# Kernel optimization log

Hardware: AMD Instinct MI355X
Metric: run time of the kernel (lower is better)

Reference implementation:

```python
import jax, jax.numpy as jnp
import numpy as np

B, N, D = 4, 1024, 1024
NH = 16
HS = D // NH
HID = 4 * D
EPS = 1e-5

def layernorm(x, w, b):
    mu = jnp.mean(x, axis=-1, keepdims=True)
    var = jnp.mean(jnp.square(x - mu), axis=-1, keepdims=True)
    return (x - mu) * jax.lax.rsqrt(var + EPS) * w + b

def setup_inputs() -> dict:
    key = jax.random.key(0)
    ks = jax.random.split(key, 8)
    s = lambda fan_in: 1.0 / np.sqrt(fan_in)
    return {
        "x": jax.random.normal(ks[0], (B, N, D), jnp.float32),
        "qkv_w": jax.random.uniform(ks[1], (3 * D, D), jnp.float32, -s(D), s(D)),
        "proj_w": jax.random.uniform(ks[2], (D, D), jnp.float32, -s(D), s(D)),
        "proj_b": jax.random.uniform(ks[3], (D,), jnp.float32, -s(D), s(D)),
        "ln1_w": jnp.ones((D,), jnp.float32),
        "ln1_b": jnp.zeros((D,), jnp.float32),
        "fc1_w": jax.random.uniform(ks[4], (HID, D), jnp.float32, -s(D), s(D)),
        "fc1_b": jax.random.uniform(ks[5], (HID,), jnp.float32, -s(D), s(D)),
        "fc2_w": jax.random.uniform(ks[6], (D, HID), jnp.float32, -s(HID), s(HID)),
        "fc2_b": jax.random.uniform(ks[7], (D,), jnp.float32, -s(HID), s(HID)),
        "ln2_w": jnp.ones((D,), jnp.float32),
        "ln2_b": jnp.zeros((D,), jnp.float32),
    }

def attention(x, qkv_w, proj_w, proj_b):
    # x: [b, n, d]; qkv linear (no bias), split into q,k,v per head
    qkv = jnp.einsum('bnd,ed->bne', x, qkv_w)              # [b, n, 3d]
    qkv = qkv.reshape(B, N, 3, NH, HS).transpose(2, 0, 3, 1, 4)  # [3, b, nh, n, hs]
    q, k, v = qkv[0], qkv[1], qkv[2]
    scale = HS ** -0.5
    # mask=False => self.mask == 1, so (mask-1)*LARGE_NUMBER == 0
    att = jax.nn.softmax(scale * jnp.einsum('bhqe,bhke->bhqk', q, k), axis=-1)
    y = jnp.einsum('bhqk,bhke->bhqe', att, v)              # [b, nh, n, hs]
    y = y.transpose(0, 2, 1, 3).reshape(B, N, D)
    return jnp.einsum('bnd,ed->bne', y, proj_w) + proj_b

def mlp(x, fc1_w, fc1_b, fc2_w, fc2_b):
    h = jax.nn.gelu(jnp.einsum('bnd,hd->bnh', x, fc1_w) + fc1_b, approximate=False)
    return jnp.einsum('bnh,dh->bnd', h, fc2_w) + fc2_b

def reference(x, qkv_w, proj_w, proj_b, ln1_w, ln1_b, fc1_w, fc1_b, fc2_w, fc2_b, ln2_w, ln2_b):
    x = x + attention(layernorm(x, ln1_w, ln1_b), qkv_w, proj_w, proj_b)
    x = x + mlp(layernorm(x, ln2_w, ln2_b), fc1_w, fc1_b, fc2_w, fc2_b)
    return x
```

## Files before the change

kernel.cpp:

```cpp
#include <hip/hip_runtime.h>
#include <hip/hip_bf16.h>

typedef __attribute__((ext_vector_type(8))) short short8;
typedef __attribute__((ext_vector_type(8))) unsigned short ushort8;
typedef __attribute__((ext_vector_type(4))) float floatx4;

#define DEV static __device__ __forceinline__

DEV unsigned short f2bf(float f) {
  unsigned int u = __builtin_bit_cast(unsigned int, f);
  u += 0x7fff + ((u >> 16) & 1);
  return (unsigned short)(u >> 16);
}
DEV float bf2f(unsigned short u) {
  return __builtin_bit_cast(float, (unsigned int)u << 16);
}
DEV unsigned int cvtpk_bf16(float lo, float hi) {
  unsigned int r;
  asm("v_cvt_pk_bf16_f32 %0, %1, %2" : "=v"(r) : "v"(lo), "v"(hi));
  return r;
}

DEV void gload_lds16(const void* g, void* l) {
  __builtin_amdgcn_global_load_lds(
      (const __attribute__((address_space(1))) unsigned int*)g,
      (__attribute__((address_space(3))) unsigned int*)l, 16, 0, 0);
}

__global__ __launch_bounds__(256) void cvt4_kernel(const float* __restrict__ w0,
                                                   const float* __restrict__ w1,
                                                   const float* __restrict__ w2,
                                                   const float* __restrict__ w3,
                                                   unsigned short* __restrict__ o0,
                                                   unsigned short* __restrict__ o1,
                                                   unsigned short* __restrict__ o2,
                                                   unsigned short* __restrict__ o3) {
  int i = blockIdx.x * 256 + threadIdx.x;
  const float* in; unsigned short* out; int j;
  if (i < 786432)       { in = w0; out = o0; j = i; }
  else if (i < 1048576) { in = w1; out = o1; j = i - 786432; }
  else if (i < 2097152) { in = w2; out = o2; j = i - 1048576; }
  else                  { in = w3; out = o3; j = i - 2097152; }
  float4 v = reinterpret_cast<const float4*>(in)[j];
  ushort4 o;
  o.x = f2bf(v.x); o.y = f2bf(v.y); o.z = f2bf(v.z); o.w = f2bf(v.w);
  reinterpret_cast<ushort4*>(out)[j] = o;
}

__global__ __launch_bounds__(256) void ln_kernel(const float* __restrict__ x,
                                                 const float* __restrict__ w,
                                                 const float* __restrict__ b,
                                                 unsigned short* __restrict__ out) {
  const int row = blockIdx.x;
  const float* xr = x + (size_t)row * 1024;
  float4 v = reinterpret_cast<const float4*>(xr)[threadIdx.x];
  float s  = v.x + v.y + v.z + v.w;
  float ss = v.x*v.x + v.y*v.y + v.z*v.z + v.w*v.w;
  #pragma unroll
  for (int off = 1; off < 64; off <<= 1) {
    s  += __shfl_xor(s, off);
    ss += __shfl_xor(ss, off);
  }
  __shared__ float red[8];
  const int wid = threadIdx.x >> 6, lane = threadIdx.x & 63;
  if (lane == 0) { red[wid] = s; red[4 + wid] = ss; }
  __syncthreads();
  s  = red[0] + red[1] + red[2] + red[3];
  ss = red[4] + red[5] + red[6] + red[7];
  const float mu  = s * (1.0f / 1024.0f);
  const float var = ss * (1.0f / 1024.0f) - mu * mu;
  const float rstd = rsqrtf(var + 1e-5f);
  float4 wv = reinterpret_cast<const float4*>(w)[threadIdx.x];
  float4 bv = reinterpret_cast<const float4*>(b)[threadIdx.x];
  ushort4 o;
  o.x = f2bf((v.x - mu) * rstd * wv.x + bv.x);
  o.y = f2bf((v.y - mu) * rstd * wv.y + bv.y);
  o.z = f2bf((v.z - mu) * rstd * wv.z + bv.z);
  o.w = f2bf((v.w - mu) * rstd * wv.w + bv.w);
  reinterpret_cast<ushort4*>(out)[(size_t)row * 256 + threadIdx.x] = o;
}

template<int EPI>
__global__ __launch_bounds__(512, 2) void gemm256(const unsigned short* __restrict__ A,
                                                  const unsigned short* __restrict__ Bw,
                                                  unsigned short* __restrict__ outb,
                                                  const float* __restrict__ bias,
                                                  int K, int N, int NT) {
  __shared__ unsigned short As[2][256 * 64];
  __shared__ unsigned short Bs[2][256 * 64];
  const int tid = threadIdx.x, lane = tid & 63, wid = tid >> 6;
  const int wr = wid >> 2, wc = wid & 3;
  const int fr = lane & 15, s0 = lane >> 4;

  const int nwg = gridDim.x;
  const int qq = nwg >> 3, rr8 = nwg & 7, xcd = blockIdx.x & 7, lid = blockIdx.x >> 3;
  const int wg = (xcd < rr8 ? xcd * (qq + 1) : rr8 * (qq + 1) + (xcd - rr8) * qq) + lid;
  const int brow = (wg / NT) * 256, bcol = (wg % NT) * 256;

  const unsigned short* ag[4];
  const unsigned short* bg[4];
  #pragma unroll
  for (int L = 0; L < 4; L++) {
    const int idx = L * 512 + tid;
    const int row = idx >> 3;
    const int ss  = ((idx & 7) ^ (row & 7)) * 8;
    ag[L] = A  + (size_t)(brow + row) * K + ss;
    bg[L] = Bw + (size_t)(bcol + row) * K + ss;
  }
  const int ldst = tid * 8;

  #define STG256(kt, buf)                                                     \
    do {                                                                      \
      const int ko = (kt) * 64;                                               \
      gload_lds16(ag[0] + ko, &As[buf][ldst]);                                \
      gload_lds16(ag[1] + ko, &As[buf][4096 + ldst]);                         \
      gload_lds16(ag[2] + ko, &As[buf][8192 + ldst]);                         \
      gload_lds16(ag[3] + ko, &As[buf][12288 + ldst]);                        \
      gload_lds16(bg[0] + ko, &Bs[buf][ldst]);                                \
      gload_lds16(bg[1] + ko, &Bs[buf][4096 + ldst]);                         \
      gload_lds16(bg[2] + ko, &Bs[buf][8192 + ldst]);                         \
      gload_lds16(bg[3] + ko, &Bs[buf][12288 + ldst]);                        \
    } while (0)

  const int xs = fr & 7;
  const int aoff = (wr * 128 + fr) * 64;
  const int boff = (wc * 64 + fr) * 64;
  const int sl0 = ((0 + s0) ^ xs) * 8;
  const int sl1 = ((4 + s0) ^ xs) * 8;

  floatx4 acc[8][4];
  #pragma unroll
  for (int m = 0; m < 8; m++)
    #pragma unroll
    for (int n = 0; n < 4; n++) acc[m][n] = (floatx4){0.f, 0.f, 0.f, 0.f};

  const int NTK = K >> 6;
  STG256(0, 0);

  for (int kt = 0; kt < NTK; ++kt) {
    const int cur = kt & 1;
    if (kt + 1 < NTK) {
      STG256(kt + 1, cur ^ 1);
      asm volatile("s_waitcnt vmcnt(8)" ::: "memory");
    } else {
      asm volatile("s_waitcnt vmcnt(0)" ::: "memory");
    }
    __builtin_amdgcn_s_barrier();

    const unsigned short* Ac = As[cur];
    const unsigned short* Bc = Bs[cur];
    short8 a0[4][2], a1[4][2], b0[2][2], b1[2][2];

    #pragma unroll
    for (int m = 0; m < 4; m++) {
      a0[m][0] = *reinterpret_cast<const short8*>(Ac + aoff + m * 1024 + sl0);
      a0[m][1] = *reinterpret_cast<const short8*>(Ac + aoff + m * 1024 + sl1);
    }
    #pragma unroll
    for (int n = 0; n < 2; n++) {
      b0[n][0] = *reinterpret_cast<const short8*>(Bc + boff + n * 1024 + sl0);
      b0[n][1] = *reinterpret_cast<const short8*>(Bc + boff + n * 1024 + sl1);
    }
    __builtin_amdgcn_s_barrier();
    __builtin_amdgcn_s_setprio(1);
    #pragma unroll
    for (int m = 0; m < 4; m++)
      #pragma unroll
      for (int n = 0; n < 2; n++) {
        acc[m][n] = __builtin_amdgcn_mfma_f32_16x16x32_bf16(a0[m][0], b0[n][0], acc[m][n], 0, 0, 0);
        acc[m][n] = __builtin_amdgcn_mfma_f32_16x16x32_bf16(a0[m][1], b0[n][1], acc[m][n], 0, 0, 0);
      }
    __builtin_amdgcn_s_setprio(0);
    __builtin_amdgcn_s_barrier();

    #pragma unroll
    for (int n = 0; n < 2; n++) {
      b1[n][0] = *reinterpret_cast<const short8*>(Bc + boff + (n + 2) * 1024 + sl0);
      b1[n][1] = *reinterpret_cast<const short8*>(Bc + boff + (n + 2) * 1024 + sl1);
    }
    __builtin_amdgcn_s_barrier();
    __builtin_amdgcn_s_setprio(1);
    #pragma unroll
    for (int m = 0; m < 4; m++)
      #pragma unroll
      for (int n = 0; n < 2; n++) {
        acc[m][n + 2] = __builtin_amdgcn_mfma_f32_16x16x32_bf16(a0[m][0], b1[n][0], acc[m][n + 2], 0, 0, 0);
        acc[m][n + 2] = __builtin_amdgcn_mfma_f32_16x16x32_bf16(a0[m][1], b1[n][1], acc[m][n + 2], 0, 0, 0);
      }
    __builtin_amdgcn_s_setprio(0);
    __builtin_amdgcn_s_barrier();

    #pragma unroll
    for (int m = 0; m < 4; m++) {
      a1[m][0] = *reinterpret_cast<const short8*>(Ac + aoff + (m + 4) * 1024 + sl0);
      a1[m][1] = *reinterpret_cast<const short8*>(Ac + aoff + (m + 4) * 1024 + sl1);
    }
    __builtin_amdgcn_s_barrier();
    __builtin_amdgcn_s_setprio(1);
    #pragma unroll
    for (int m = 0; m < 4; m++)
      #pragma unroll
      for (int n = 0; n < 2; n++) {
        acc[m + 4][n] = __builtin_amdgcn_mfma_f32_16x16x32_bf16(a1[m][0], b0[n][0], acc[m + 4][n], 0, 0, 0);
        acc[m + 4][n] = __builtin_amdgcn_mfma_f32_16x16x32_bf16(a1[m][1], b0[n][1], acc[m + 4][n], 0, 0, 0);
      }
    __builtin_amdgcn_s_setprio(0);
    __builtin_amdgcn_s_barrier();

    __builtin_amdgcn_s_setprio(1);
    #pragma unroll
    for (int m = 0; m < 4; m++)
      #pragma unroll
      for (int n = 0; n < 2; n++) {
        acc[m + 4][n + 2] = __builtin_amdgcn_mfma_f32_16x16x32_bf16(a1[m][0], b1[n][0], acc[m + 4][n + 2], 0, 0, 0);
        acc[m + 4][n + 2] = __builtin_amdgcn_mfma_f32_16x16x32_bf16(a1[m][1], b1[n][1], acc[m + 4][n + 2], 0, 0, 0);
      }
    __builtin_amdgcn_s_setprio(0);
    __builtin_amdgcn_s_barrier();
  }
  #undef STG256

  #pragma unroll
  for (int m = 0; m < 8; m++) {
    #pragma unroll
    for (int n = 0; n < 4; n++) {
      const int col = bcol + wc * 64 + n * 16 + fr;
      #pragma unroll
      for (int r = 0; r < 4; r++) {
        const size_t idx = (size_t)(brow + wr * 128 + m * 16 + s0 * 4 + r) * N + col;
        float v = acc[m][n][r];
        if (EPI == 1) {
          v += bias[col];
          const float u = v * 0.7978845608f * (1.0f + 0.044715f * v * v);
          const float e = __expf(2.0f * u);
          v = v * (e / (e + 1.0f));
        }
        outb[idx] = f2bf(v);
      }
    }
  }
}

__global__ __launch_bounds__(512) void gemm128sk(const unsigned short* __restrict__ A,
                                                 const unsigned short* __restrict__ Bw,
                                                 unsigned short* __restrict__ outb,
                                                 int K, int Ksl, int N, int NT, int ntiles) {
  __shared__ unsigned short As[4][128 * 32];
  __shared__ unsigned short Bs[4][128 * 32];
  const int tid = threadIdx.x, lane = tid & 63, wid = tid >> 6;
  const int wrow = (wid >> 2) * 64, wcol = (wid & 3) * 32;
  const int fr = lane & 15, s0 = lane >> 4;

  const int nwg = gridDim.x;
  const int qq = nwg >> 3, rr8 = nwg & 7, xcd = blockIdx.x & 7, lid = blockIdx.x >> 3;
  const int wg = (xcd < rr8 ? xcd * (qq + 1) : rr8 * (qq + 1) + (xcd - rr8) * qq) + lid;
  const int kslice = wg / ntiles, t = wg % ntiles;
  const int brow = (t / NT) * 128, bcol = (t % NT) * 128;
  const int kofs = kslice * Ksl;

  const int srow = tid >> 2;
  const int sslot = ((tid & 3) ^ ((srow >> 1) & 3)) * 8;
  const unsigned short* ag = A  + (size_t)(brow + srow) * K + kofs + sslot;
  const unsigned short* bg = Bw + (size_t)(bcol + srow) * K + kofs + sslot;
  const int ldst = tid * 8;

  #define STG(kt, buf)                              \
    do {                                            \
      const int ko = (kt) * 32;                     \
      gload_lds16(ag + ko, &As[buf][ldst]);         \
      gload_lds16(bg + ko, &Bs[buf][ldst]);         \
    } while (0)

  const int slr = (s0 ^ ((fr >> 1) & 3)) * 8;

  floatx4 acc[4][2];
  #pragma unroll
  for (int i = 0; i < 4; i++)
    #pragma unroll
    for (int j = 0; j < 2; j++) acc[i][j] = (floatx4){0.f, 0.f, 0.f, 0.f};

  const int NTK = Ksl >> 5;
  STG(0, 0);
  STG(1, 1);
  STG(2, 2);

  for (int kt = 0; kt < NTK; ++kt) {
    const int cur = kt & 3;
    if (kt + 3 < NTK) {
      STG(kt + 3, (kt + 3) & 3);
      asm volatile("s_waitcnt vmcnt(6)" ::: "memory");
    } else if (kt + 2 < NTK) {
      asm volatile("s_waitcnt vmcnt(4)" ::: "memory");
    } else if (kt + 1 < NTK) {
      asm volatile("s_waitcnt vmcnt(2)" ::: "memory");
    } else {
      asm volatile("s_waitcnt vmcnt(0)" ::: "memory");
    }
    __builtin_amdgcn_s_barrier();

    short8 af[4], bf[2];
    #pragma unroll
    for (int i = 0; i < 4; i++)
      af[i] = *reinterpret_cast<const short8*>(&As[cur][(wrow + i * 16 + fr) * 32 + slr]);
    #pragma unroll
    for (int j = 0; j < 2; j++)
      bf[j] = *reinterpret_cast<const short8*>(&Bs[cur][(wcol + j * 16 + fr) * 32 + slr]);
    __builtin_amdgcn_s_setprio(1);
    #pragma unroll
    for (int i = 0; i < 4; i++)
      #pragma unroll
      for (int j = 0; j < 2; j++)
        acc[i][j] = __builtin_amdgcn_mfma_f32_16x16x32_bf16(af[i], bf[j], acc[i][j], 0, 0, 0);
    __builtin_amdgcn_s_setprio(0);
    __builtin_amdgcn_s_barrier();
  }
  #undef STG

  unsigned short* po = outb + (size_t)kslice * ((size_t)ntiles * 16384);
  const int erow = brow + wrow + (s0 << 2);
  const int ecol = bcol + wcol + fr;
  #pragma unroll
  for (int i = 0; i < 4; i++)
    #pragma unroll
    for (int j = 0; j < 2; j++)
      #pragma unroll
      for (int r = 0; r < 4; r++)
        po[(size_t)(erow + i * 16 + r) * N + ecol + j * 16] = f2bf(acc[i][j][r]);
}

__global__ __launch_bounds__(256) void red_ln(const unsigned short* __restrict__ p0,
                                              const unsigned short* __restrict__ p1,
                                              const float* __restrict__ x,
                                              const float* __restrict__ bias,
                                              const float* __restrict__ lw,
                                              const float* __restrict__ lb,
                                              float* __restrict__ x1,
                                              unsigned short* __restrict__ xn) {
  const int row = blockIdx.x, t = threadIdx.x;
  const size_t o4 = (size_t)row * 256 + t;
  ushort4 a = reinterpret_cast<const ushort4*>(p0)[o4];
  ushort4 c = reinterpret_cast<const ushort4*>(p1)[o4];
  float4 xv = reinterpret_cast<const float4*>(x)[o4];
  float4 bv = reinterpret_cast<const float4*>(bias)[t];
  float4 v;
  v.x = bf2f(a.x) + bf2f(c.x) + bv.x + xv.x;
  v.y = bf2f(a.y) + bf2f(c.y) + bv.y + xv.y;
  v.z = bf2f(a.z) + bf2f(c.z) + bv.z + xv.z;
  v.w = bf2f(a.w) + bf2f(c.w) + bv.w + xv.w;
  reinterpret_cast<float4*>(x1)[o4] = v;

  float s  = v.x + v.y + v.z + v.w;
  float ss = v.x*v.x + v.y*v.y + v.z*v.z + v.w*v.w;
  #pragma unroll
  for (int off = 1; off < 64; off <<= 1) {
    s  += __shfl_xor(s, off);
    ss += __shfl_xor(ss, off);
  }
  __shared__ float red[8];
  const int wid = t >> 6, lane = t & 63;
  if (lane == 0) { red[wid] = s; red[4 + wid] = ss; }
  __syncthreads();
  s  = red[0] + red[1] + red[2] + red[3];
  ss = red[4] + red[5] + red[6] + red[7];
  const float mu  = s * (1.0f / 1024.0f);
  const float var = ss * (1.0f / 1024.0f) - mu * mu;
  const float rstd = rsqrtf(var + 1e-5f);
  float4 wv = reinterpret_cast<const float4*>(lw)[t];
  float4 lv = reinterpret_cast<const float4*>(lb)[t];
  ushort4 o;
  o.x = f2bf((v.x - mu) * rstd * wv.x + lv.x);
  o.y = f2bf((v.y - mu) * rstd * wv.y + lv.y);
  o.z = f2bf((v.z - mu) * rstd * wv.z + lv.z);
  o.w = f2bf((v.w - mu) * rstd * wv.w + lv.w);
  reinterpret_cast<ushort4*>(xn)[o4] = o;
}

__global__ __launch_bounds__(256) void red_out(const unsigned short* __restrict__ p0,
                                               const unsigned short* __restrict__ p1,
                                               const float* __restrict__ x1,
                                               const float* __restrict__ bias,
                                               float* __restrict__ out) {
  const size_t i4 = (size_t)blockIdx.x * 256 + threadIdx.x;
  const int c4 = (int)(i4 & 255);
  ushort4 a = reinterpret_cast<const ushort4*>(p0)[i4];
  ushort4 c = reinterpret_cast<const ushort4*>(p1)[i4];
  float4 xv = reinterpret_cast<const float4*>(x1)[i4];
  float4 bv = reinterpret_cast<const float4*>(bias)[c4];
  float4 v;
  v.x = bf2f(a.x) + bf2f(c.x) + bv.x + xv.x;
  v.y = bf2f(a.y) + bf2f(c.y) + bv.y + xv.y;
  v.z = bf2f(a.z) + bf2f(c.z) + bv.z + xv.z;
  v.w = bf2f(a.w) + bf2f(c.w) + bv.w + xv.w;
  reinterpret_cast<float4*>(out)[i4] = v;
}

__global__ __launch_bounds__(256) void vtrans_kernel(const unsigned short* __restrict__ qkv,
                                                     unsigned short* __restrict__ vt) {
  __shared__ unsigned short T[64][66];
  const int nt = blockIdx.x, bh = blockIdx.y;
  const int b = bh >> 4, h = bh & 15;
  const unsigned short* src = qkv + (size_t)b * 1024 * 3072 + 2048 + h * 64;
  const int r = threadIdx.x >> 3, s = threadIdx.x & 7;
  ushort8 a0 = *reinterpret_cast<const ushort8*>(src + (size_t)(nt * 64 + r) * 3072 + s * 8);
  ushort8 a1 = *reinterpret_cast<const ushort8*>(src + (size_t)(nt * 64 + r + 32) * 3072 + s * 8);
  #pragma unroll
  for (int j = 0; j < 8; j++) {
    T[r][s * 8 + j]      = a0[j];
    T[r + 32][s * 8 + j] = a1[j];
  }
  __syncthreads();
  ushort8 o0, o1;
  #pragma unroll
  for (int j = 0; j < 8; j++) {
    o0[j] = T[s * 8 + j][r];
    o1[j] = T[s * 8 + j][r + 32];
  }
  unsigned short* dst = vt + (size_t)bh * 64 * 1024 + nt * 64 + s * 8;
  *reinterpret_cast<ushort8*>(dst + (size_t)r * 1024)        = o0;
  *reinterpret_cast<ushort8*>(dst + (size_t)(r + 32) * 1024) = o1;
}

__global__ __launch_bounds__(512) void attn_kernel(const unsigned short* __restrict__ qkv,
                                                   const unsigned short* __restrict__ vt,
                                                   unsigned short* __restrict__ y) {
  __shared__ unsigned short Ks[2][64 * 64];
  __shared__ unsigned short Vs[2][64 * 64];
  __shared__ unsigned long long Pq[8][256];

  const int tid = threadIdx.x;
  const int lane = tid & 63;
  const int w = tid >> 6;
  const int wg = (blockIdx.x & 7) * 64 + (blockIdx.x >> 3);
  const int bh = wg >> 3, qt = wg & 7;
  const int b = bh >> 4, h = bh & 15;
  const int fr = lane & 15, s0 = lane >> 4;
  const int sw = fr & 7;
  const size_t RS = 3072;

  const unsigned short* qbase = qkv + (size_t)b * 1024 * RS + h * 64;
  const unsigned short* kbase = qbase + 1024;
  const unsigned short* vbase = vt + (size_t)bh * 64 * 1024;

  const float SC = 0.125f * 1.44269504089f;

  short8 aq[2];
  {
    const unsigned short* qrow = qbase + (size_t)(qt * 128 + w * 16 + fr) * RS;
    ushort8 q0 = *reinterpret_cast<const ushort8*>(qrow + s0 * 8);
    ushort8 q1 = *reinterpret_cast<const ushort8*>(qrow + 32 + s0 * 8);
    #pragma unroll
    for (int i = 0; i < 8; i++) {
      q0[i] = f2bf(bf2f(q0[i]) * SC);
      q1[i] = f2bf(bf2f(q1[i]) * SC);
    }
    aq[0] = __builtin_bit_cast(short8, q0);
    aq[1] = __builtin_bit_cast(short8, q1);
  }

  float m_run = -1e30f, l_run = 0.f;
  floatx4 accy[4];
  #pragma unroll
  for (int d = 0; d < 4; d++) accy[d] = (floatx4){0.f, 0.f, 0.f, 0.f};

  const int krow = tid >> 3, kslot = tid & 7;
  const int gslot = (kslot ^ (krow & 7)) * 8;
  const unsigned short* kg = kbase + (size_t)krow * RS + gslot;
  const unsigned short* vg = vbase + (size_t)krow * 1024 + gslot;

  #define STAGE(t, buf)                                           \
    do {                                                          \
      gload_lds16(kg + (size_t)(t) * 64 * RS, &Ks[buf][tid * 8]); \
      gload_lds16(vg + (size_t)(t) * 64,      &Vs[buf][tid * 8]); \
    } while (0)

  STAGE(0, 0);
  int cur = 0;

  for (int kt = 0; kt < 16; ++kt) {
    if (kt < 15) {
      STAGE(kt + 1, cur ^ 1);
      asm volatile("s_waitcnt vmcnt(2)" ::: "memory");
    } else {
      asm volatile("s_waitcnt vmcnt(0)" ::: "memory");
    }
    __builtin_amdgcn_s_barrier();

    const unsigned short* Kt = Ks[cur];
    const unsigned short* Vc = Vs[cur];

    floatx4 st[4];
    __builtin_amdgcn_s_setprio(1);
    #pragma unroll
    for (int f = 0; f < 4; ++f) {
      const unsigned short* krw = Kt + (f * 16 + fr) * 64;
      short8 kb0 = *reinterpret_cast<const short8*>(krw + (((s0)     ^ sw) << 3));
      short8 kb1 = *reinterpret_cast<const short8*>(krw + (((s0 + 4) ^ sw) << 3));
      floatx4 s = (floatx4){0.f, 0.f, 0.f, 0.f};
      s = __builtin_amdgcn_mfma_f32_16x16x32_bf16(kb0, aq[0], s, 0, 0, 0);
      s = __builtin_amdgcn_mfma_f32_16x16x32_bf16(kb1, aq[1], s, 0, 0, 0);
      st[f] = s;
    }
    __builtin_amdgcn_s_setprio(0);

    float pm;
    {
      float m0 = fmaxf(fmaxf(st[0][0], st[0][1]), fmaxf(st[0][2], st[0][3]));
      float m1 = fmaxf(fmaxf(st[1][0], st[1][1]), fmaxf(st[1][2], st[1][3]));
      float m2 = fmaxf(fmaxf(st[2][0], st[2][1]), fmaxf(st[2][2], st[2][3]));
      float m3 = fmaxf(fmaxf(st[3][0], st[3][1]), fmaxf(st[3][2], st[3][3]));
      pm = fmaxf(fmaxf(m0, m1), fmaxf(m2, m3));
      pm = fmaxf(pm, __shfl_xor(pm, 16));
      pm = fmaxf(pm, __shfl_xor(pm, 32));
    }
    if (__any(pm > m_run + 8.f)) {
      const float mn = fmaxf(m_run, pm);
      const float alpha = exp2f(m_run - mn);
      m_run = mn;
      l_run *= alpha;
      float a0 = __shfl(alpha, s0 * 4 + 0);
      float a1 = __shfl(alpha, s0 * 4 + 1);
      float a2 = __shfl(alpha, s0 * 4 + 2);
      float a3 = __shfl(alpha, s0 * 4 + 3);
      #pragma unroll
      for (int j = 0; j < 4; j++) {
        accy[j][0] *= a0; accy[j][1] *= a1; accy[j][2] *= a2; accy[j][3] *= a3;
      }
    }

    float ps = 0.f;
    unsigned long long pk[4];
    #pragma unroll
    for (int f = 0; f < 4; f++) {
      float p0 = exp2f(st[f][0] - m_run);
      float p1 = exp2f(st[f][1] - m_run);
      float p2 = exp2f(st[f][2] - m_run);
      float p3 = exp2f(st[f][3] - m_run);
      ps += (p0 + p1) + (p2 + p3);
      unsigned int lo = cvtpk_bf16(p0, p1);
      unsigned int hi = cvtpk_bf16(p2, p3);
      pk[f] = (unsigned long long)lo | ((unsigned long long)hi << 32);
    }
    ps += __shfl_xor(ps, 16);
    ps += __shfl_xor(ps, 32);
    l_run += ps;

    #pragma unroll
    for (int f = 0; f < 4; f++)
      Pq[w][(f * 4 + s0) * 16 + (fr ^ (s0 << 2))] = pk[f];

    __builtin_amdgcn_s_setprio(1);
    #pragma unroll
    for (int ks = 0; ks < 2; ++ks) {
      const int b0 = ks * 8 + s0 * 2, b1 = b0 + 1;
      unsigned long long q0 = Pq[w][b0 * 16 + (fr ^ ((b0 & 3) << 2))];
      unsigned long long q1 = Pq[w][b1 * 16 + (fr ^ ((b1 & 3) << 2))];
      ulonglong2 u; u.x = q0; u.y = q1;
      short8 ap = __builtin_bit_cast(short8, u);
      const int sA = ((ks * 4 + s0) ^ sw) << 3;
      #pragma unroll
      for (int j = 0; j < 4; ++j) {
        short8 vb = *reinterpret_cast<const short8*>(Vc + (j * 16 + fr) * 64 + sA);
        accy[j] = __builtin_amdgcn_mfma_f32_16x16x32_bf16(ap, vb, accy[j], 0, 0, 0);
      }
    }
    __builtin_amdgcn_s_setprio(0);
    __builtin_amdgcn_s_barrier();
    cur ^= 1;
  }
  #undef STAGE

  float linv[4];
  #pragma unroll
  for (int r = 0; r < 4; r++) linv[r] = 1.0f / __shfl(l_run, s0 * 4 + r);
  #pragma unroll
  for (int r = 0; r < 4; r++) {
    const size_t grow2 =
        (size_t)(b * 1024 + qt * 128 + w * 16 + s0 * 4 + r) * 1024 + h * 64;
    #pragma unroll
    for (int j = 0; j < 4; ++j)
      y[grow2 + j * 16 + fr] = f2bf(accy[j][r] * linv[r]);
  }
}

extern "C" void kernel_launch(void* const* d_in, const int* in_sizes, int n_in,
                              void* d_out, int out_size, void* d_ws, size_t ws_size,
                              hipStream_t stream) {
  const float* x      = (const float*)d_in[0];
  const float* qkv_w  = (const float*)d_in[1];
  const float* proj_w = (const float*)d_in[2];
  const float* proj_b = (const float*)d_in[3];
  const float* ln1_w  = (const float*)d_in[4];
  const float* ln1_b  = (const float*)d_in[5];
  const float* fc1_w  = (const float*)d_in[6];
  const float* fc1_b  = (const float*)d_in[7];
  const float* fc2_w  = (const float*)d_in[8];
  const float* fc2_b  = (const float*)d_in[9];
  const float* ln2_w  = (const float*)d_in[10];
  const float* ln2_b  = (const float*)d_in[11];
  float* out = (float*)d_out;

  char* ws = (char*)d_ws;
  unsigned short* qkvw16  = (unsigned short*)(ws + 0);
  unsigned short* projw16 = (unsigned short*)(ws + 6291456);
  unsigned short* fc1w16  = (unsigned short*)(ws + 8388608);
  unsigned short* fc2w16  = (unsigned short*)(ws + 16777216);
  float*          x1      = (float*)(ws + 25165824);
  unsigned short* vt      = (unsigned short*)(ws + 25165824);
  unsigned short* xn      = (unsigned short*)(ws + 41943040);
  unsigned short* big     = (unsigned short*)(ws + 50331648);
  unsigned short* pp      = big;
  unsigned short* fp      = (unsigned short*)(ws + 0);

  cvt4_kernel<<<12288, 256, 0, stream>>>(qkv_w, proj_w, fc1_w, fc2_w,
                                         qkvw16, projw16, fc1w16, fc2w16);

  ln_kernel<<<4096, 256, 0, stream>>>(x, ln1_w, ln1_b, xn);
  gemm256<0><<<192, 512, 0, stream>>>(xn, qkvw16, big, nullptr, 1024, 3072, 12);
  vtrans_kernel<<<dim3(16, 64), 256, 0, stream>>>(big, vt);
  attn_kernel<<<512, 512, 0, stream>>>(big, vt, xn);
  gemm128sk<<<512, 512, 0, stream>>>(xn, projw16, pp, 1024, 512, 1024, 8, 256);
  red_ln<<<4096, 256, 0, stream>>>(pp, pp + 4194304, x, proj_b, ln2_w, ln2_b, x1, xn);
  gemm256<1><<<256, 512, 0, stream>>>(xn, fc1w16, big, fc1_b, 1024, 4096, 16);
  gemm128sk<<<512, 512, 0, stream>>>(big, fc2w16, fp, 4096, 2048, 1024, 8, 256);
  red_out<<<4096, 256, 0, stream>>>(fp, fp + 4194304, x1, fc2_b, out);
}
```

Measured before the change: 232.2 us.

## Issue prefetch after barrier and drop trailing barriers in GEMM and attention loops

In the big GEMM, split-K GEMM and flash-attention kernels, the next tile's global-to-LDS load is now issued after the single top-of-loop barrier, so the end-of-iteration barrier can be removed. The big GEMM also loads all B fragments at once and drops the interleaved barriers between its MFMA phases, cutting synchronisation count per k-step. The cost is less load/compute overlap in the double-buffered kernels, which now wait for vmcnt(0) before each step. Holding more fragments in registers at once may also raise register pressure.

```diff
diff --git a/kernel.cpp b/kernel.cpp
--- a/kernel.cpp
+++ b/kernel.cpp
@@ -139,84 +139,47 @@
 
   for (int kt = 0; kt < NTK; ++kt) {
     const int cur = kt & 1;
-    if (kt + 1 < NTK) {
-      STG256(kt + 1, cur ^ 1);
-      asm volatile("s_waitcnt vmcnt(8)" ::: "memory");
-    } else {
-      asm volatile("s_waitcnt vmcnt(0)" ::: "memory");
-    }
+    asm volatile("s_waitcnt vmcnt(0)" ::: "memory");
     __builtin_amdgcn_s_barrier();
+    if (kt + 1 < NTK) STG256(kt + 1, cur ^ 1);
 
     const unsigned short* Ac = As[cur];
     const unsigned short* Bc = Bs[cur];
-    short8 a0[4][2], a1[4][2], b0[2][2], b1[2][2];
-
+    short8 bfv[4][2], a0[4][2], a1[4][2];
+
+    #pragma unroll
+    for (int n = 0; n < 4; n++) {
+      bfv[n][0] = *reinterpret_cast<const short8*>(Bc + boff + n * 1024 + sl0);
+      bfv[n][1] = *reinterpret_cast<const short8*>(Bc + boff + n * 1024 + sl1);
+    }
     #pragma unroll
     for (int m = 0; m < 4; m++) {
       a0[m][0] = *reinterpret_cast<const short8*>(Ac + aoff + m * 1024 + sl0);
       a0[m][1] = *reinterpret_cast<const short8*>(Ac + aoff + m * 1024 + sl1);
     }
-    #pragma unroll
-    for (int n = 0; n < 2; n++) {
-      b0[n][0] = *reinterpret_cast<const short8*>(Bc + boff + n * 1024 + sl0);
-      b0[n][1] = *reinterpret_cast<const short8*>(Bc + boff + n * 1024 + sl1);
-    }
-    __builtin_amdgcn_s_barrier();
     __builtin_amdgcn_s_setprio(1);
     #pragma unroll
     for (int m = 0; m < 4; m++)
       #pragma unroll
-      for (int n = 0; n < 2; n++) {
-        acc[m][n] = __builtin_amdgcn_mfma_f32_16x16x32_bf16(a0[m][0], b0[n][0], acc[m][n], 0, 0, 0);
-        acc[m][n] = __builtin_amdgcn_mfma_f32_16x16x32_bf16(a0[m][1], b0[n][1], acc[m][n], 0, 0, 0);
+      for (int n = 0; n < 4; n++) {
+        acc[m][n] = __builtin_amdgcn_mfma_f32_16x16x32_bf16(a0[m][0], bfv[n][0], acc[m][n], 0, 0, 0);
+        acc[m][n] = __builtin_amdgcn_mfma_f32_16x16x32_bf16(a0[m][1], bfv[n][1], acc[m][n], 0, 0, 0);
       }
     __builtin_amdgcn_s_setprio(0);
-    __builtin_amdgcn_s_barrier();
-
-    #pragma unroll
-    for (int n = 0; n < 2; n++) {
-      b1[n][0] = *reinterpret_cast<const short8*>(Bc + boff + (n + 2) * 1024 + sl0);
-      b1[n][1] = *reinterpret_cast<const short8*>(Bc + boff + (n + 2) * 1024 + sl1);
-    }
-    __builtin_amdgcn_s_barrier();
-    __builtin_amdgcn_s_setprio(1);
-    #pragma unroll
-    for (int m = 0; m < 4; m++)
-      #pragma unroll
-      for (int n = 0; n < 2; n++) {
-        acc[m][n + 2] = __builtin_amdgcn_mfma_f32_16x16x32_bf16(a0[m][0], b1[n][0], acc[m][n + 2], 0, 0, 0);
-        acc[m][n + 2] = __builtin_amdgcn_mfma_f32_16x16x32_bf16(a0[m][1], b1[n][1], acc[m][n + 2], 0, 0, 0);
-      }
-    __builtin_amdgcn_s_setprio(0);
-    __builtin_amdgcn_s_barrier();
-
     #pragma unroll
     for (int m = 0; m < 4; m++) {
       a1[m][0] = *reinterpret_cast<const short8*>(Ac + aoff + (m + 4) * 1024 + sl0);
       a1[m][1] = *reinterpret_cast<const short8*>(Ac + aoff + (m + 4) * 1024 + sl1);
     }
-    __builtin_amdgcn_s_barrier();
     __builtin_amdgcn_s_setprio(1);
     #pragma unroll
     for (int m = 0; m < 4; m++)
       #pragma unroll
-      for (int n = 0; n < 2; n++) {
-        acc[m + 4][n] = __builtin_amdgcn_mfma_f32_16x16x32_bf16(a1[m][0], b0[n][0], acc[m + 4][n], 0, 0, 0);
-        acc[m + 4][n] = __builtin_amdgcn_mfma_f32_16x16x32_bf16(a1[m][1], b0[n][1], acc[m + 4][n], 0, 0, 0);
+      for (int n = 0; n < 4; n++) {
+        acc[m + 4][n] = __builtin_amdgcn_mfma_f32_16x16x32_bf16(a1[m][0], bfv[n][0], acc[m + 4][n], 0, 0, 0);
+        acc[m + 4][n] = __builtin_amdgcn_mfma_f32_16x16x32_bf16(a1[m][1], bfv[n][1], acc[m + 4][n], 0, 0, 0);
       }
     __builtin_amdgcn_s_setprio(0);
-    __builtin_amdgcn_s_barrier();
-
-    __builtin_amdgcn_s_setprio(1);
-    #pragma unroll
-    for (int m = 0; m < 4; m++)
-      #pragma unroll
-      for (int n = 0; n < 2; n++) {
-        acc[m + 4][n + 2] = __builtin_amdgcn_mfma_f32_16x16x32_bf16(a1[m][0], b1[n][0], acc[m + 4][n + 2], 0, 0, 0);
-        acc[m + 4][n + 2] = __builtin_amdgcn_mfma_f32_16x16x32_bf16(a1[m][1], b1[n][1], acc[m + 4][n + 2], 0, 0, 0);
-      }
-    __builtin_amdgcn_s_setprio(0);
-    __builtin_amdgcn_s_barrier();
   }
   #undef STG256
 
@@ -286,17 +249,15 @@
 
   for (int kt = 0; kt < NTK; ++kt) {
     const int cur = kt & 3;
-    if (kt + 3 < NTK) {
-      STG(kt + 3, (kt + 3) & 3);
-      asm volatile("s_waitcnt vmcnt(6)" ::: "memory");
-    } else if (kt + 2 < NTK) {
+    if (kt < NTK - 2) {
       asm volatile("s_waitcnt vmcnt(4)" ::: "memory");
-    } else if (kt + 1 < NTK) {
+    } else if (kt == NTK - 2) {
       asm volatile("s_waitcnt vmcnt(2)" ::: "memory");
     } else {
       asm volatile("s_waitcnt vmcnt(0)" ::: "memory");
     }
     __builtin_amdgcn_s_barrier();
+    if (kt + 3 < NTK) STG(kt + 3, (kt + 3) & 3);
 
     short8 af[4], bf[2];
     #pragma unroll
@@ -312,7 +273,6 @@
       for (int j = 0; j < 2; j++)
         acc[i][j] = __builtin_amdgcn_mfma_f32_16x16x32_bf16(af[i], bf[j], acc[i][j], 0, 0, 0);
     __builtin_amdgcn_s_setprio(0);
-    __builtin_amdgcn_s_barrier();
   }
   #undef STG
 
@@ -477,13 +437,9 @@
   int cur = 0;
 
   for (int kt = 0; kt < 16; ++kt) {
-    if (kt < 15) {
-      STAGE(kt + 1, cur ^ 1);
-      asm volatile("s_waitcnt vmcnt(2)" ::: "memory");
-    } else {
-      asm volatile("s_waitcnt vmcnt(0)" ::: "memory");
-    }
+    asm volatile("s_waitcnt vmcnt(0)" ::: "memory");
     __builtin_amdgcn_s_barrier();
+    if (kt < 15) STAGE(kt + 1, cur ^ 1);
 
     const unsigned short* Kt = Ks[cur];
     const unsigned short* Vc = Vs[cur];
@@ -564,7 +520,6 @@
       }
     }
     __builtin_amdgcn_s_setprio(0);
-    __builtin_amdgcn_s_barrier();
     cur ^= 1;
   }
   #undef STAGE
```

Result: faster. 222.5 us (-4.2%).
